# Kernel tuning notes

Measured on AMD Instinct MI355X. Metric: run time of the kernel, lower is better.

Reference implementation:

```python
import jax, jax.numpy as jnp
from jax import lax
import numpy as np

B, T, V, U = 64, 2048, 256, 256
BLANK = 0
NEG = jnp.float32(-1e30)


def setup_inputs() -> dict:
    key = jax.random.key(0)
    k1, k2, k3, k4 = jax.random.split(key, 4)
    logits = jax.random.normal(k1, (B, T, V), dtype=jnp.float32)
    targets = jax.random.randint(k2, (B, U), 1, V)               # labels 1..V-1 (0 = blank)
    targets_lengths = jax.random.randint(k3, (B,), U // 2, U + 1)
    logits_lengths = jax.random.randint(k4, (B,), T // 2, T + 1)
    return dict(logits=logits, targets=targets,
                logits_lengths=logits_lengths, targets_lengths=targets_lengths)


def _ctc_forced_alignment(logp, targets, logits_lengths, targets_lengths):
    """Viterbi forced alignment over the CTC extended state graph.
    Returns per-frame best-path labels, shape [B, T] (get_alignment_3d, is_ctc=True)."""
    Bs, Ts, _ = logp.shape
    Us = targets.shape[1]
    S = 2 * Us + 1
    s_idx = jnp.arange(S)
    # extended sequence: blank, t1, blank, t2, ..., blank
    lab_pos = jnp.minimum(s_idx // 2, Us - 1)
    ext = jnp.where((s_idx % 2 == 1)[None, :], jnp.take(targets, lab_pos, axis=1), BLANK)  # [B,S]
    # emission scores em[b,t,s] = logp[b,t,ext[b,s]]
    em = jnp.take_along_axis(logp, jnp.broadcast_to(ext[:, None, :], (Bs, Ts, S)), axis=2)

    valid = s_idx[None, :] < (2 * targets_lengths[:, None] + 1)              # [B,S]
    ext_m2 = jnp.pad(ext[:, :-2], ((0, 0), (2, 0)), constant_values=BLANK)
    skip_ok = (s_idx[None, :] >= 2) & ((s_idx % 2 == 1)[None, :]) & (ext != ext_m2)

    idx_blank = 2 * targets_lengths          # last blank state (S_b - 1)
    idx_label = 2 * targets_lengths - 1      # last label state (S_b - 2)

    alpha0 = jnp.where(valid & (s_idx[None, :] <= 1), em[:, 0, :], NEG)

    def pair_of(alpha):
        vb = jnp.take_along_axis(alpha, idx_blank[:, None], axis=1)
        vl = jnp.take_along_axis(alpha, idx_label[:, None], axis=1)
        return jnp.concatenate([vb, vl], axis=1)  # [B,2]

    def step(alpha, em_t):
        a1 = jnp.pad(alpha[:, :-1], ((0, 0), (1, 0)), constant_values=NEG)
        a2 = jnp.where(skip_ok, jnp.pad(alpha[:, :-2], ((0, 0), (2, 0)), constant_values=NEG), NEG)
        stacked = jnp.stack([alpha, a1, a2])     # [3,B,S]
        bp = jnp.argmax(stacked, axis=0).astype(jnp.int32)
        alpha_new = jnp.where(valid, jnp.max(stacked, axis=0) + em_t, NEG)
        return alpha_new, (bp, pair_of(alpha_new))

    _, (bps, pairs) = lax.scan(step, alpha0, jnp.moveaxis(em, 1, 0)[1:])
    bps = jnp.concatenate([jnp.zeros((1, Bs, S), jnp.int32), bps])            # [T,B,S]
    pairs = jnp.concatenate([pair_of(alpha0)[None], pairs])                   # [T,B,2]

    last_pair = pairs[logits_lengths - 1, jnp.arange(Bs)]                     # value at final valid frame
    end_state = jnp.where(last_pair[:, 0] >= last_pair[:, 1], idx_blank, idx_label).astype(jnp.int32)

    def back(s, inp):
        t, bp_t = inp
        label = jnp.take_along_axis(ext, s[:, None], axis=1)[:, 0]
        step_bp = jnp.take_along_axis(bp_t, s[:, None], axis=1)[:, 0]
        s_prev = jnp.where(t - 1 >= logits_lengths - 1, end_state, s - step_bp)
        return s_prev.astype(jnp.int32), label

    ts = jnp.arange(Ts - 1, -1, -1)
    _, labels_rev = lax.scan(back, end_state, (ts, bps[::-1]))
    return labels_rev[::-1].T  # [B,T] per-frame aligned target labels


def reference(logits, targets, logits_lengths, targets_lengths):
    logp = jax.nn.log_softmax(logits, axis=2)                                 # [B,T,V]
    aligned = lax.stop_gradient(
        _ctc_forced_alignment(logp, targets, logits_lengths, targets_lengths))
    nll = -jnp.take_along_axis(logp, aligned[:, :, None], axis=2)[..., 0]     # [B,T]
    mask = (jnp.arange(logp.shape[1])[None, :] < logits_lengths[:, None]).astype(logp.dtype)
    # reduce=True: mean over valid (unmasked) positions
    return jnp.sum(nll * mask) / jnp.sum(mask)
```

## Files before the change

### kernel.cpp

```cpp
#include <hip/hip_runtime.h>

#define NEGF -1e30f
typedef unsigned int uint32;

static constexpr int Bb = 64, Tt = 2048, Vv = 256, Uu = 256;

__device__ __forceinline__ unsigned short f2bf(float f) {
  uint32 u = __builtin_bit_cast(uint32, f);
  u += 0x7fffu + ((u >> 16) & 1u);
  return (unsigned short)(u >> 16);
}
__device__ __forceinline__ float bf2f_lo(uint32 p) { return __builtin_bit_cast(float, p << 16); }
__device__ __forceinline__ float bf2f_hi(uint32 p) { return __builtin_bit_cast(float, p & 0xffff0000u); }

__device__ __forceinline__ float dpp_shr1(float old, float src) {
  return __builtin_bit_cast(float, __builtin_amdgcn_update_dpp(
      __builtin_bit_cast(int, old), __builtin_bit_cast(int, src), 0x138, 0xF, 0xF, false));
}
__device__ __forceinline__ float dpp_shl1(float old, float src) {
  return __builtin_bit_cast(float, __builtin_amdgcn_update_dpp(
      __builtin_bit_cast(int, old), __builtin_bit_cast(int, src), 0x130, 0xF, 0xF, false));
}

__global__ __launch_bounds__(256) void gather_lse_kernel(
    const float* __restrict__ logits, const int* __restrict__ targets,
    const int* __restrict__ llen, float* __restrict__ gpart,
    float* __restrict__ Ebs, unsigned short* __restrict__ E) {
  __shared__ __align__(16) float buf[4][8][Vv];
  __shared__ float wpart[4];
  const int b = blockIdx.x >> 5;
  const int c = blockIdx.x & 31;
  const int w = threadIdx.x >> 6;
  const int lane = threadIdx.x & 63;
  const int L = llen[b];
  const int4 lb = reinterpret_cast<const int4*>(targets + (b << 8))[lane];
  const float* __restrict__ lgb = logits + (size_t)b * (Tt * Vv);
  float lse_local = 0.f;
#pragma unroll
  for (int k = 0; k < 2; ++k) {
    const int tbase = (c << 6) + (k << 5) + w;
    if (tbase >= L) break;
    float4 v[8];
#pragma unroll
    for (int j = 0; j < 8; ++j)
      v[j] = reinterpret_cast<const float4*>(lgb + (size_t)(tbase + 4 * j) * Vv)[lane];
    float s[8];
#pragma unroll
    for (int j = 0; j < 8; ++j)
      s[j] = __expf(v[j].x) + __expf(v[j].y) + __expf(v[j].z) + __expf(v[j].w);
#pragma unroll
    for (int off = 32; off; off >>= 1) {
#pragma unroll
      for (int j = 0; j < 8; ++j) s[j] += __shfl_down(s[j], off);
    }
#pragma unroll
    for (int j = 0; j < 8; ++j)
      reinterpret_cast<float4*>(&buf[w][j][0])[lane] = v[j];
#pragma unroll
    for (int j = 0; j < 8; ++j) {
      const int t = tbase + 4 * j;
      const bool val = t < L;
      ushort4 o;
      o.x = f2bf(buf[w][j][lb.x]); o.y = f2bf(buf[w][j][lb.y]);
      o.z = f2bf(buf[w][j][lb.z]); o.w = f2bf(buf[w][j][lb.w]);
      if (val)
        reinterpret_cast<ushort4*>(E + ((size_t)((b << 11) + t)) * Vv)[lane] = o;
      if ((lane == 0) & val) {
        lse_local += __logf(s[j]);
        Ebs[(b << 11) + ((t == 0) ? 2047 : t - 1)] = v[j].x;
      }
    }
  }
  if (lane == 0) wpart[w] = lse_local;
  __syncthreads();
  if (threadIdx.x == 0)
    gpart[blockIdx.x] = wpart[0] + wpart[1] + wpart[2] + wpart[3];
}

#define PG 8
__global__ __launch_bounds__(128) void viterbi_kernel(
    const unsigned short* __restrict__ E, const float* __restrict__ Ebs,
    const int* __restrict__ targets, const int* __restrict__ llen,
    const int* __restrict__ tlen, float* __restrict__ vpart) {
  __shared__ __align__(16) float LB[2048];
  __shared__ float Bt[520];
  const int b = blockIdx.x;
  const int lane = threadIdx.x & 63;
  const int wv = threadIdx.x >> 6;
  const int L = llen[b];
  const int tl = tlen[b];
  const int M = (L - 2) >> 1;
  const int4 lb = reinterpret_cast<const int4*>(targets + (b << 8))[lane];
  const uint2* __restrict__ Erow = reinterpret_cast<const uint2*>(E) + ((size_t)(b << 11) << 6);
  const float* __restrict__ Ebb = Ebs + (b << 11);

  {
    const float4* src = reinterpret_cast<const float4*>(Ebb);
    float4* dst = reinterpret_cast<float4*>(LB);
    for (int i = threadIdx.x; i < 512; i += 128) dst[i] = src[i];
  }
  __syncthreads();

  float a0 = NEGF, a1 = NEGF, a2 = NEGF, a3 = NEGF, a4 = NEGF,
        a5 = NEGF, a6 = NEGF, a7 = NEGF, a8 = NEGF;

  if (wv == 0) {
    const int prevw = __shfl_up(lb.w, 1);
    const bool sk0 = (lane != 0) && (lb.x != prevw);
    const bool sk1 = (lb.y != lb.x);
    const bool sk2 = (lb.z != lb.y);
    const bool sk3 = (lb.w != lb.z);
    if (lane == 0) {
      a0 = LB[2047];
      a1 = bf2f_lo((uint32)*reinterpret_cast<const unsigned short*>(E + ((size_t)(b << 11) << 8)));
    }
    uint2 pf[PG][4];
    float4 pb[PG];
    auto fetchf = [&](int slot, int k) {
      const int kk = (k > 511) ? 511 : k;
#pragma unroll
      for (int j = 0; j < 4; ++j) {
        int r = 1 + 4 * kk + j; r = (r > 2047) ? 2047 : r;
        pf[slot][j] = Erow[(size_t)(r << 6) + lane];
      }
      pb[slot] = reinterpret_cast<const float4*>(LB)[kk];
    };
    auto stepf = [&](uint2 em, float eb) {
      const float e0 = bf2f_lo(em.x), e1 = bf2f_hi(em.x);
      const float e2 = bf2f_lo(em.y), e3 = bf2f_hi(em.y);
      const float am1 = dpp_shr1(NEGF, a7);
      const float x0 = fmaxf(a0, am1) + eb;
      const float x1 = fmaxf(fmaxf(a1, a0), sk0 ? am1 : NEGF) + e0;
      const float x2 = fmaxf(a2, a1) + eb;
      const float x3 = fmaxf(fmaxf(a3, a2), sk1 ? a1 : NEGF) + e1;
      const float x4 = fmaxf(a4, a3) + eb;
      const float x5 = fmaxf(fmaxf(a5, a4), sk2 ? a3 : NEGF) + e2;
      const float x6 = fmaxf(a6, a5) + eb;
      const float x7 = fmaxf(fmaxf(a7, a6), sk3 ? a5 : NEGF) + e3;
      const float x8 = fmaxf(a8, a7) + eb;
      a0 = x0; a1 = x1; a2 = x2; a3 = x3; a4 = x4; a5 = x5; a6 = x6; a7 = x7; a8 = x8;
    };
    const int n = M, Gf = n >> 2, remf = n & 3;
#pragma unroll
    for (int s = 0; s < PG; ++s) fetchf(s, s);
    __builtin_amdgcn_sched_barrier(0);
    int g = 0;
    while (g + PG <= Gf) {
#pragma unroll
      for (int s = 0; s < PG; ++s) {
#pragma unroll
        for (int j = 0; j < 4; ++j) stepf(pf[s][j], (&pb[s].x)[j]);
        fetchf(s, g + s + PG);
        __builtin_amdgcn_sched_barrier(0);
      }
      g += PG;
    }
    const int left = Gf - g;
#pragma unroll
    for (int s = 0; s < PG; ++s) {
      if (s < left) {
#pragma unroll
        for (int j = 0; j < 4; ++j) stepf(pf[s][j], (&pb[s].x)[j]);
      }
    }
#pragma unroll
    for (int s = 0; s < PG; ++s) {
      if (s == left) {
#pragma unroll
        for (int j = 0; j < 4; ++j)
          if (j < remf) stepf(pf[s][j], (&pb[s].x)[j]);
      }
    }
  } else {
    const int nlabx = __shfl_down(lb.x, 1);
    const bool kb0 = (lb.y != lb.x);
    const bool kb1 = (lb.z != lb.y);
    const bool kb2 = (lb.w != lb.z);
    const bool kb3 = (lane < 63) && (nlabx != lb.w);
    {
      const uint2 er = Erow[(size_t)((L - 1) << 6) + lane];
      const float e0 = bf2f_lo(er.x), e1 = bf2f_hi(er.x);
      const float e2 = bf2f_lo(er.y), e3 = bf2f_hi(er.y);
      const float blankL = LB[L - 2];
      const int s0 = 8 * lane, tb = 2 * tl, tm = 2 * tl - 1;
      a0 = (s0     == tb) ? blankL : NEGF;
      a1 = (s0 + 1 == tm) ? e0     : NEGF;
      a2 = (s0 + 2 == tb) ? blankL : NEGF;
      a3 = (s0 + 3 == tm) ? e1     : NEGF;
      a4 = (s0 + 4 == tb) ? blankL : NEGF;
      a5 = (s0 + 5 == tm) ? e2     : NEGF;
      a6 = (s0 + 6 == tb) ? blankL : NEGF;
      a7 = (s0 + 7 == tm) ? e3     : NEGF;
      a8 = ((lane == 63) && (tb == 512)) ? blankL : NEGF;
    }
    uint2 qf[PG][4];
    float qb[PG][4];
    auto fetchb = [&](int slot, int k) {
#pragma unroll
      for (int j = 0; j < 4; ++j) {
        int r = L - 2 - 4 * k - j; r = (r < 1) ? 1 : r;
        qf[slot][j] = Erow[(size_t)(r << 6) + lane];
        qb[slot][j] = LB[r - 1];
      }
    };
    auto stepb = [&](uint2 em, float eb) {
      const float e0 = bf2f_lo(em.x), e1 = bf2f_hi(em.x);
      const float e2 = bf2f_lo(em.y), e3 = bf2f_hi(em.y);
      const float bn0 = dpp_shl1(a8, a0);
      const float bn1 = dpp_shl1(NEGF, a1);
      const float y0 = fmaxf(a0, a1) + eb;
      const float y1 = fmaxf(fmaxf(a1, a2), kb0 ? a3 : NEGF) + e0;
      const float y2 = fmaxf(a2, a3) + eb;
      const float y3 = fmaxf(fmaxf(a3, a4), kb1 ? a5 : NEGF) + e1;
      const float y4 = fmaxf(a4, a5) + eb;
      const float y5 = fmaxf(fmaxf(a5, a6), kb2 ? a7 : NEGF) + e2;
      const float y6 = fmaxf(a6, a7) + eb;
      const float y7 = fmaxf(fmaxf(a7, bn0), kb3 ? bn1 : NEGF) + e3;
      const float y8 = a8 + eb;
      a0 = y0; a1 = y1; a2 = y2; a3 = y3; a4 = y4; a5 = y5; a6 = y6; a7 = y7; a8 = y8;
    };
    const int n = L - 2 - M, Gb = n >> 2, remb = n & 3;
#pragma unroll
    for (int s = 0; s < PG; ++s) fetchb(s, s);
    __builtin_amdgcn_sched_barrier(0);
    int g = 0;
    while (g + PG <= Gb) {
#pragma unroll
      for (int s = 0; s < PG; ++s) {
#pragma unroll
        for (int j = 0; j < 4; ++j) stepb(qf[s][j], qb[s][j]);
        fetchb(s, g + s + PG);
        __builtin_amdgcn_sched_barrier(0);
      }
      g += PG;
    }
    const int left = Gb - g;
#pragma unroll
    for (int s = 0; s < PG; ++s) {
      if (s < left) {
#pragma unroll
        for (int j = 0; j < 4; ++j) stepb(qf[s][j], qb[s][j]);
      }
    }
#pragma unroll
    for (int s = 0; s < PG; ++s) {
      if (s == left) {
#pragma unroll
        for (int j = 0; j < 4; ++j)
          if (j < remb) stepb(qf[s][j], qb[s][j]);
      }
    }
    Bt[8 * lane + 0] = a0; Bt[8 * lane + 1] = a1;
    Bt[8 * lane + 2] = a2; Bt[8 * lane + 3] = a3;
    Bt[8 * lane + 4] = a4; Bt[8 * lane + 5] = a5;
    Bt[8 * lane + 6] = a6; Bt[8 * lane + 7] = a7;
    if (lane == 63) Bt[512] = a8;
    if (lane == 0) { Bt[513] = NEGF; Bt[514] = NEGF; }
  }
  __syncthreads();
  if (wv == 0) {
    const int nlabx = __shfl_down(lb.x, 1);
    const bool kb0 = (lb.y != lb.x);
    const bool kb1 = (lb.z != lb.y);
    const bool kb2 = (lb.w != lb.z);
    const bool kb3 = (lane < 63) && (nlabx != lb.w);
    const int s0 = 8 * lane;
    float best;
    best =             a0 + fmaxf(Bt[s0],     Bt[s0 + 1]);
    best = fmaxf(best, a1 + fmaxf(fmaxf(Bt[s0 + 1], Bt[s0 + 2]), kb0 ? Bt[s0 + 3] : NEGF));
    best = fmaxf(best, a2 + fmaxf(Bt[s0 + 2], Bt[s0 + 3]));
    best = fmaxf(best, a3 + fmaxf(fmaxf(Bt[s0 + 3], Bt[s0 + 4]), kb1 ? Bt[s0 + 5] : NEGF));
    best = fmaxf(best, a4 + fmaxf(Bt[s0 + 4], Bt[s0 + 5]));
    best = fmaxf(best, a5 + fmaxf(fmaxf(Bt[s0 + 5], Bt[s0 + 6]), kb2 ? Bt[s0 + 7] : NEGF));
    best = fmaxf(best, a6 + fmaxf(Bt[s0 + 6], Bt[s0 + 7]));
    best = fmaxf(best, a7 + fmaxf(fmaxf(Bt[s0 + 7], Bt[s0 + 8]), kb3 ? Bt[s0 + 9] : NEGF));
    best = fmaxf(best, a8 + Bt[512]);
#pragma unroll
    for (int off = 32; off; off >>= 1) best = fmaxf(best, __shfl_down(best, off));
    if (lane == 0) vpart[b] = best;
  }
}

__global__ __launch_bounds__(256) void finalize_kernel(
    const int* __restrict__ llen, const float* __restrict__ gpart,
    const float* __restrict__ vpart, float* __restrict__ out) {
  __shared__ float sred[4], lred[4];
  const int t = threadIdx.x, lane = t & 63, w = t >> 6;
  float s = 0.f;
#pragma unroll
  for (int i = 0; i < 8; ++i) s += gpart[t + (i << 8)];
  float lf = 0.f;
  if (t < 64) { s -= vpart[t]; lf = (float)llen[t]; }
#pragma unroll
  for (int off = 32; off; off >>= 1) {
    s += __shfl_down(s, off);
    lf += __shfl_down(lf, off);
  }
  if (lane == 0) { sred[w] = s; lred[w] = lf; }
  __syncthreads();
  if (t == 0)
    out[0] = (sred[0] + sred[1] + sred[2] + sred[3]) /
             (lred[0] + lred[1] + lred[2] + lred[3]);
}

extern "C" void kernel_launch(void* const* d_in, const int* in_sizes, int n_in,
                              void* d_out, int out_size, void* d_ws, size_t ws_size,
                              hipStream_t stream) {
  const float* logits  = (const float*)d_in[0];
  const int*   targets = (const int*)d_in[1];
  const int*   llen    = (const int*)d_in[2];
  const int*   tlen    = (const int*)d_in[3];
  float* out = (float*)d_out;

  float*          gpart = (float*)d_ws;
  float*          vpart = (float*)d_ws + 2048;
  float*          Ebs   = (float*)((char*)d_ws + 16384);
  unsigned short* E     = (unsigned short*)((char*)d_ws + (1u << 20));

  gather_lse_kernel<<<Bb * 32, 256, 0, stream>>>(logits, targets, llen, gpart, Ebs, E);
  viterbi_kernel<<<Bb, 128, 0, stream>>>(E, Ebs, targets, llen, tlen, vpart);
  finalize_kernel<<<1, 256, 0, stream>>>(llen, gpart, vpart, out);
}
```

Measured before the change: 275.8 us.

## Normalize emissions by frame blank score to drop blank adds from Viterbi recurrence

The gather kernel now stores each label emission relative to that frame's blank log-prob, so blank states in the forward and backward Viterbi recurrences need no per-step add and no per-frame blank load from shared memory. The constant offset is restored afterwards by summing the blank scores across valid frames and adding that sum to the best path value. This takes an add and an LDS load off the serial dependency chain per step, at the cost of a small reduction at the end and bf16 rounding now applied to the difference instead of the raw value.

```diff
diff --git a/kernel.cpp b/kernel.cpp
--- a/kernel.cpp
+++ b/kernel.cpp
@@ -60,9 +60,10 @@
     for (int j = 0; j < 8; ++j) {
       const int t = tbase + 4 * j;
       const bool val = t < L;
+      const float bl = buf[w][j][0];
       ushort4 o;
-      o.x = f2bf(buf[w][j][lb.x]); o.y = f2bf(buf[w][j][lb.y]);
-      o.z = f2bf(buf[w][j][lb.z]); o.w = f2bf(buf[w][j][lb.w]);
+      o.x = f2bf(buf[w][j][lb.x] - bl); o.y = f2bf(buf[w][j][lb.y] - bl);
+      o.z = f2bf(buf[w][j][lb.z] - bl); o.w = f2bf(buf[w][j][lb.w] - bl);
       if (val)
         reinterpret_cast<ushort4*>(E + ((size_t)((b << 11) + t)) * Vv)[lane] = o;
       if ((lane == 0) & val) {
@@ -111,11 +112,10 @@
     const bool sk2 = (lb.z != lb.y);
     const bool sk3 = (lb.w != lb.z);
     if (lane == 0) {
-      a0 = LB[2047];
+      a0 = 0.f;
       a1 = bf2f_lo((uint32)*reinterpret_cast<const unsigned short*>(E + ((size_t)(b << 11) << 8)));
     }
     uint2 pf[PG][4];
-    float4 pb[PG];
     auto fetchf = [&](int slot, int k) {
       const int kk = (k > 511) ? 511 : k;
 #pragma unroll
@@ -123,21 +123,20 @@
         int r = 1 + 4 * kk + j; r = (r > 2047) ? 2047 : r;
         pf[slot][j] = Erow[(size_t)(r << 6) + lane];
       }
-      pb[slot] = reinterpret_cast<const float4*>(LB)[kk];
     };
-    auto stepf = [&](uint2 em, float eb) {
+    auto stepf = [&](uint2 em) {
       const float e0 = bf2f_lo(em.x), e1 = bf2f_hi(em.x);
       const float e2 = bf2f_lo(em.y), e3 = bf2f_hi(em.y);
       const float am1 = dpp_shr1(NEGF, a7);
-      const float x0 = fmaxf(a0, am1) + eb;
+      const float x0 = fmaxf(a0, am1);
       const float x1 = fmaxf(fmaxf(a1, a0), sk0 ? am1 : NEGF) + e0;
-      const float x2 = fmaxf(a2, a1) + eb;
+      const float x2 = fmaxf(a2, a1);
       const float x3 = fmaxf(fmaxf(a3, a2), sk1 ? a1 : NEGF) + e1;
-      const float x4 = fmaxf(a4, a3) + eb;
+      const float x4 = fmaxf(a4, a3);
       const float x5 = fmaxf(fmaxf(a5, a4), sk2 ? a3 : NEGF) + e2;
-      const float x6 = fmaxf(a6, a5) + eb;
+      const float x6 = fmaxf(a6, a5);
       const float x7 = fmaxf(fmaxf(a7, a6), sk3 ? a5 : NEGF) + e3;
-      const float x8 = fmaxf(a8, a7) + eb;
+      const float x8 = fmaxf(a8, a7);
       a0 = x0; a1 = x1; a2 = x2; a3 = x3; a4 = x4; a5 = x5; a6 = x6; a7 = x7; a8 = x8;
     };
     const int n = M, Gf = n >> 2, remf = n & 3;
@@ -149,7 +148,7 @@
 #pragma unroll
       for (int s = 0; s < PG; ++s) {
 #pragma unroll
-        for (int j = 0; j < 4; ++j) stepf(pf[s][j], (&pb[s].x)[j]);
+        for (int j = 0; j < 4; ++j) stepf(pf[s][j]);
         fetchf(s, g + s + PG);
         __builtin_amdgcn_sched_barrier(0);
       }
@@ -160,7 +159,7 @@
     for (int s = 0; s < PG; ++s) {
       if (s < left) {
 #pragma unroll
-        for (int j = 0; j < 4; ++j) stepf(pf[s][j], (&pb[s].x)[j]);
+        for (int j = 0; j < 4; ++j) stepf(pf[s][j]);
       }
     }
 #pragma unroll
@@ -168,7 +167,7 @@
       if (s == left) {
 #pragma unroll
         for (int j = 0; j < 4; ++j)
-          if (j < remf) stepf(pf[s][j], (&pb[s].x)[j]);
+          if (j < remf) stepf(pf[s][j]);
       }
     }
   } else {
@@ -181,43 +180,39 @@
       const uint2 er = Erow[(size_t)((L - 1) << 6) + lane];
       const float e0 = bf2f_lo(er.x), e1 = bf2f_hi(er.x);
       const float e2 = bf2f_lo(er.y), e3 = bf2f_hi(er.y);
-      const float blankL = LB[L - 2];
       const int s0 = 8 * lane, tb = 2 * tl, tm = 2 * tl - 1;
-      a0 = (s0     == tb) ? blankL : NEGF;
-      a1 = (s0 + 1 == tm) ? e0     : NEGF;
-      a2 = (s0 + 2 == tb) ? blankL : NEGF;
-      a3 = (s0 + 3 == tm) ? e1     : NEGF;
-      a4 = (s0 + 4 == tb) ? blankL : NEGF;
-      a5 = (s0 + 5 == tm) ? e2     : NEGF;
-      a6 = (s0 + 6 == tb) ? blankL : NEGF;
-      a7 = (s0 + 7 == tm) ? e3     : NEGF;
-      a8 = ((lane == 63) && (tb == 512)) ? blankL : NEGF;
+      a0 = (s0     == tb) ? 0.f : NEGF;
+      a1 = (s0 + 1 == tm) ? e0  : NEGF;
+      a2 = (s0 + 2 == tb) ? 0.f : NEGF;
+      a3 = (s0 + 3 == tm) ? e1  : NEGF;
+      a4 = (s0 + 4 == tb) ? 0.f : NEGF;
+      a5 = (s0 + 5 == tm) ? e2  : NEGF;
+      a6 = (s0 + 6 == tb) ? 0.f : NEGF;
+      a7 = (s0 + 7 == tm) ? e3  : NEGF;
+      a8 = ((lane == 63) && (tb == 512)) ? 0.f : NEGF;
     }
     uint2 qf[PG][4];
-    float qb[PG][4];
     auto fetchb = [&](int slot, int k) {
 #pragma unroll
       for (int j = 0; j < 4; ++j) {
         int r = L - 2 - 4 * k - j; r = (r < 1) ? 1 : r;
         qf[slot][j] = Erow[(size_t)(r << 6) + lane];
-        qb[slot][j] = LB[r - 1];
       }
     };
-    auto stepb = [&](uint2 em, float eb) {
+    auto stepb = [&](uint2 em) {
       const float e0 = bf2f_lo(em.x), e1 = bf2f_hi(em.x);
       const float e2 = bf2f_lo(em.y), e3 = bf2f_hi(em.y);
       const float bn0 = dpp_shl1(a8, a0);
       const float bn1 = dpp_shl1(NEGF, a1);
-      const float y0 = fmaxf(a0, a1) + eb;
+      const float y0 = fmaxf(a0, a1);
       const float y1 = fmaxf(fmaxf(a1, a2), kb0 ? a3 : NEGF) + e0;
-      const float y2 = fmaxf(a2, a3) + eb;
+      const float y2 = fmaxf(a2, a3);
       const float y3 = fmaxf(fmaxf(a3, a4), kb1 ? a5 : NEGF) + e1;
-      const float y4 = fmaxf(a4, a5) + eb;
+      const float y4 = fmaxf(a4, a5);
       const float y5 = fmaxf(fmaxf(a5, a6), kb2 ? a7 : NEGF) + e2;
-      const float y6 = fmaxf(a6, a7) + eb;
+      const float y6 = fmaxf(a6, a7);
       const float y7 = fmaxf(fmaxf(a7, bn0), kb3 ? bn1 : NEGF) + e3;
-      const float y8 = a8 + eb;
-      a0 = y0; a1 = y1; a2 = y2; a3 = y3; a4 = y4; a5 = y5; a6 = y6; a7 = y7; a8 = y8;
+      a0 = y0; a1 = y1; a2 = y2; a3 = y3; a4 = y4; a5 = y5; a6 = y6; a7 = y7;
     };
     const int n = L - 2 - M, Gb = n >> 2, remb = n & 3;
 #pragma unroll
@@ -228,7 +223,7 @@
 #pragma unroll
       for (int s = 0; s < PG; ++s) {
 #pragma unroll
-        for (int j = 0; j < 4; ++j) stepb(qf[s][j], qb[s][j]);
+        for (int j = 0; j < 4; ++j) stepb(qf[s][j]);
         fetchb(s, g + s + PG);
         __builtin_amdgcn_sched_barrier(0);
       }
@@ -239,7 +234,7 @@
     for (int s = 0; s < PG; ++s) {
       if (s < left) {
 #pragma unroll
-        for (int j = 0; j < 4; ++j) stepb(qf[s][j], qb[s][j]);
+        for (int j = 0; j < 4; ++j) stepb(qf[s][j]);
       }
     }
 #pragma unroll
@@ -247,7 +242,7 @@
       if (s == left) {
 #pragma unroll
         for (int j = 0; j < 4; ++j)
-          if (j < remb) stepb(qf[s][j], qb[s][j]);
+          if (j < remb) stepb(qf[s][j]);
       }
     }
     Bt[8 * lane + 0] = a0; Bt[8 * lane + 1] = a1;
@@ -275,9 +270,18 @@
     best = fmaxf(best, a6 + fmaxf(Bt[s0 + 6], Bt[s0 + 7]));
     best = fmaxf(best, a7 + fmaxf(fmaxf(Bt[s0 + 7], Bt[s0 + 8]), kb3 ? Bt[s0 + 9] : NEGF));
     best = fmaxf(best, a8 + Bt[512]);
-#pragma unroll
-    for (int off = 32; off; off >>= 1) best = fmaxf(best, __shfl_down(best, off));
-    if (lane == 0) vpart[b] = best;
+    float csum = 0.f;
+#pragma unroll
+    for (int i = 0; i < 32; ++i) {
+      const int idx = lane + (i << 6);
+      csum += (idx <= L - 2) ? LB[idx] : 0.f;
+    }
+#pragma unroll
+    for (int off = 32; off; off >>= 1) {
+      best = fmaxf(best, __shfl_down(best, off));
+      csum += __shfl_down(csum, off);
+    }
+    if (lane == 0) vpart[b] = best + csum + LB[2047];
   }
 }
 
```

Measured after the change: 260.4 us. 1.06x faster.
